# Kernel tuning notes

Measured on AMD Instinct MI355X. Metric: run time of the kernel, lower is better.

The kernel has to match this reference:

```python
import jax, jax.numpy as jnp
import numpy as np

B, H, S, D = 2, 16, 2048, 128


def setup_inputs() -> dict:
    key = jax.random.key(0)
    kq, kk, kv = jax.random.split(key, 3)
    q = jax.random.normal(kq, (B, H, S, D), dtype=jnp.float32)
    k = jax.random.normal(kk, (B, H, S, D), dtype=jnp.float32)
    v = jax.random.normal(kv, (B, H, S, D), dtype=jnp.float32)
    return {"q": q, "k": k, "v": v}


def reference(q, k, v):
    # cp_size == 1 path: causal scaled dot-product attention.
    # Identical math to the ring online-softmax accumulation collapsed to one step.
    d = q.shape[-1]
    scale = d ** -0.5
    scores = jnp.einsum("bhsd,bhtd->bhst", q, k) * scale  # (B,H,S,S)
    s = scores.shape[-1]
    causal_mask = jnp.tril(jnp.ones((s, s), dtype=bool))  # (S,S)
    scores = jnp.where(causal_mask, scores, -jnp.inf)
    probs = jax.nn.softmax(scores, axis=-1)
    return jnp.einsum("bhst,bhtd->bhsd", probs, v)
```

## Files before the change

### kernel.cpp

```cpp
#include <hip/hip_runtime.h>
#include <hip/hip_bf16.h>

constexpr int Bb = 2, Hh = 16, Ss = 2048, Dd = 128;
constexpr int BM = 64, BN = 64;
constexpr int NQT = Ss / BM;
constexpr float SCALE = 0.088388347648318447f * 1.4426950408889634f;

typedef __attribute__((ext_vector_type(8))) short bf16x8;
typedef __attribute__((ext_vector_type(4))) float f32x4;
typedef __attribute__((ext_vector_type(4))) int int4v;

__device__ __forceinline__ unsigned cvtpk(float lo, float hi) {
  unsigned r;
  asm("v_cvt_pk_bf16_f32 %0, %1, %2" : "=v"(r) : "v"(lo), "v"(hi));
  return r;
}
__device__ __forceinline__ float exp2hw(float x) {
  float r;
  asm("v_exp_f32 %0, %1" : "=v"(r) : "v"(x));
  return r;
}
__device__ __forceinline__ float fcomp(float4 f, int j) {
  return j == 0 ? f.x : (j == 1 ? f.y : (j == 2 ? f.z : f.w));
}

__global__ __launch_bounds__(256, 2)
void fa_fwd_kernel(const float* __restrict__ q, const float* __restrict__ k,
                   const float* __restrict__ v, float* __restrict__ out) {
  __shared__ __align__(16) char Klds[BN * 256];
  __shared__ __align__(16) char Vlds[Dd * 128];

  const int tid = threadIdx.x;
  const int wave = tid >> 6, lane = tid & 63, quad = lane >> 4, l16 = lane & 15;
  const int bid = blockIdx.x;
  const int bh = bid & 31;
  const int qt = (NQT - 1) - (bid >> 5);

  const float* qb = q + (size_t)bh * Ss * Dd;
  const float* kb = k + (size_t)bh * Ss * Dd;
  const float* vb = v + (size_t)bh * Ss * Dd;

  bf16x8 qf[4];
  {
    const float* qr = qb + (size_t)(qt * BM + wave * 16 + l16) * Dd + quad * 8;
    #pragma unroll
    for (int ks = 0; ks < 4; ++ks) {
      float4 a = *(const float4*)(qr + ks * 32);
      float4 b = *(const float4*)(qr + ks * 32 + 4);
      int4v t;
      t[0] = (int)cvtpk(a.x * SCALE, a.y * SCALE);
      t[1] = (int)cvtpk(a.z * SCALE, a.w * SCALE);
      t[2] = (int)cvtpk(b.x * SCALE, b.y * SCALE);
      t[3] = (int)cvtpk(b.z * SCALE, b.w * SCALE);
      qf[ks] = __builtin_bit_cast(bf16x8, t);
    }
  }

  const int krow0 = tid >> 4;
  const int kblk  = tid & 15;
  const int kswz  = kblk ^ krow0;
  const int vkg = tid >> 5;
  const int vdq = tid & 31;

  float4 ka[4], kc[4];
  float4 vr[8];

  auto load_tiles = [&](int kt) {
    const float* Kg = kb + (size_t)(kt * BN) * Dd + kblk * 8;
    #pragma unroll
    for (int i = 0; i < 4; ++i) {
      ka[i] = *(const float4*)(Kg + (size_t)(krow0 + 16 * i) * Dd);
      kc[i] = *(const float4*)(Kg + (size_t)(krow0 + 16 * i) * Dd + 4);
    }
    const float* Vg = vb + (size_t)(kt * BN + vkg * 8) * Dd + vdq * 4;
    #pragma unroll
    for (int r = 0; r < 8; ++r)
      vr[r] = *(const float4*)(Vg + (size_t)r * Dd);
  };

  auto stage_tiles = [&]() {
    #pragma unroll
    for (int i = 0; i < 4; ++i) {
      int4v t;
      t[0] = (int)cvtpk(ka[i].x, ka[i].y);
      t[1] = (int)cvtpk(ka[i].z, ka[i].w);
      t[2] = (int)cvtpk(kc[i].x, kc[i].y);
      t[3] = (int)cvtpk(kc[i].z, kc[i].w);
      *(int4v*)(Klds + (krow0 + 16 * i) * 256 + kswz * 16) = t;
    }
    #pragma unroll
    for (int j = 0; j < 4; ++j) {
      int d = vdq * 4 + j;
      int f7 = (d ^ (d >> 3)) & 7;
      int4v t;
      t[0] = (int)cvtpk(fcomp(vr[0], j), fcomp(vr[1], j));
      t[1] = (int)cvtpk(fcomp(vr[2], j), fcomp(vr[3], j));
      t[2] = (int)cvtpk(fcomp(vr[4], j), fcomp(vr[5], j));
      t[3] = (int)cvtpk(fcomp(vr[6], j), fcomp(vr[7], j));
      *(int4v*)(Vlds + d * 128 + (vkg ^ f7) * 16) = t;
    }
  };

  f32x4 o[8];
  #pragma unroll
  for (int i = 0; i < 8; ++i) o[i] = (f32x4)(0.0f);
  float mrow = -3.0e38f, lrow = 0.0f;

  load_tiles(0);
  stage_tiles();

  const int hi2 = quad >> 1;
  const int srcbase = (l16 + 32 * (quad & 1)) * 4;

  for (int kt = 0; kt <= qt; ++kt) {
    __syncthreads();
    const bool more = kt < qt;
    if (more) load_tiles(kt + 1);

    f32x4 acc[4];
    #pragma unroll
    for (int nt = 0; nt < 4; ++nt) acc[nt] = (f32x4)(0.0f);
    __builtin_amdgcn_s_setprio(1);
    #pragma unroll
    for (int ks = 0; ks < 4; ++ks) {
      #pragma unroll
      for (int nt = 0; nt < 4; ++nt) {
        int row = nt * 16 + l16;
        int bswz = (ks * 4 + quad) ^ l16;
        bf16x8 kf = *(const bf16x8*)(Klds + row * 256 + bswz * 16);
        acc[nt] = __builtin_amdgcn_mfma_f32_16x16x32_bf16(kf, qf[ks], acc[nt], 0, 0, 0);
      }
    }
    __builtin_amdgcn_s_setprio(0);

    if (kt == qt) {
      #pragma unroll
      for (int nt = 0; nt < 4; ++nt)
        #pragma unroll
        for (int r = 0; r < 4; ++r)
          if (nt * 16 + quad * 4 + r > wave * 16 + l16) acc[nt][r] = -1.0e30f;
    }

    float mx = acc[0][0];
    #pragma unroll
    for (int nt = 0; nt < 4; ++nt)
      #pragma unroll
      for (int r = 0; r < 4; ++r) mx = fmaxf(mx, acc[nt][r]);
    mx = fmaxf(mx, __shfl_xor(mx, 16, 64));
    mx = fmaxf(mx, __shfl_xor(mx, 32, 64));

    if (!__all(mx - mrow <= 8.0f)) {
      float mn = fmaxf(mrow, mx);
      float alpha = exp2hw(mrow - mn);
      mrow = mn;
      lrow *= alpha;
      #pragma unroll
      for (int r = 0; r < 4; ++r) {
        int src = (lane & 48) | (quad * 4 + r);
        float ar = __shfl(alpha, src, 64);
        #pragma unroll
        for (int dt = 0; dt < 8; ++dt) o[dt][r] *= ar;
      }
    }

    float rs = 0.f;
    #pragma unroll
    for (int nt = 0; nt < 4; ++nt)
      #pragma unroll
      for (int r = 0; r < 4; ++r) {
        float p = exp2hw(acc[nt][r] - mrow);
        acc[nt][r] = p; rs += p;
      }
    lrow += rs;

    unsigned pk0_0 = cvtpk(acc[0][0], acc[0][1]), pk0_1 = cvtpk(acc[0][2], acc[0][3]);
    unsigned pk1_0 = cvtpk(acc[1][0], acc[1][1]), pk1_1 = cvtpk(acc[1][2], acc[1][3]);
    unsigned pk2_0 = cvtpk(acc[2][0], acc[2][1]), pk2_1 = cvtpk(acc[2][2], acc[2][3]);
    unsigned pk3_0 = cvtpk(acc[3][0], acc[3][1]), pk3_1 = cvtpk(acc[3][2], acc[3][3]);

    bf16x8 pf[2];
    {
      int4v p0, p1;
      #pragma unroll
      for (int jp = 0; jp < 4; ++jp) {
        int srcb = srcbase + 64 * (jp >> 1);
        int a0 = __builtin_amdgcn_ds_bpermute(srcb, (int)((jp & 1) ? pk0_1 : pk0_0));
        int a1 = __builtin_amdgcn_ds_bpermute(srcb, (int)((jp & 1) ? pk1_1 : pk1_0));
        int a2 = __builtin_amdgcn_ds_bpermute(srcb, (int)((jp & 1) ? pk2_1 : pk2_0));
        int a3 = __builtin_amdgcn_ds_bpermute(srcb, (int)((jp & 1) ? pk3_1 : pk3_0));
        p0[jp] = hi2 ? a1 : a0;
        p1[jp] = hi2 ? a3 : a2;
      }
      pf[0] = __builtin_bit_cast(bf16x8, p0);
      pf[1] = __builtin_bit_cast(bf16x8, p1);
    }

    __builtin_amdgcn_s_setprio(1);
    #pragma unroll
    for (int ks2 = 0; ks2 < 2; ++ks2) {
      #pragma unroll
      for (int dt = 0; dt < 8; ++dt) {
        int row = dt * 16 + l16;
        int f7 = (row ^ (row >> 3)) & 7;
        int bswz = (ks2 * 4 + quad) ^ f7;
        bf16x8 vf = *(const bf16x8*)(Vlds + row * 128 + bswz * 16);
        o[dt] = __builtin_amdgcn_mfma_f32_16x16x32_bf16(pf[ks2], vf, o[dt], 0, 0, 0);
      }
    }
    __builtin_amdgcn_s_setprio(0);

    if (more) { __syncthreads(); stage_tiles(); }
  }

  lrow += __shfl_xor(lrow, 16, 64);
  lrow += __shfl_xor(lrow, 32, 64);
  float linv[4];
  #pragma unroll
  for (int r = 0; r < 4; ++r) {
    int src = (lane & 48) | (quad * 4 + r);
    linv[r] = 1.0f / __shfl(lrow, src, 64);
  }
  float* ob = out + ((size_t)bh * Ss + qt * BM + wave * 16) * Dd;
  #pragma unroll
  for (int dt = 0; dt < 8; ++dt)
    #pragma unroll
    for (int r = 0; r < 4; ++r)
      ob[(quad * 4 + r) * Dd + dt * 16 + l16] = o[dt][r] * linv[r];
}

extern "C" void kernel_launch(void* const* d_in, const int* in_sizes, int n_in,
                              void* d_out, int out_size, void* d_ws, size_t ws_size,
                              hipStream_t stream) {
  const float* q = (const float*)d_in[0];
  const float* k = (const float*)d_in[1];
  const float* v = (const float*)d_in[2];
  float* out = (float*)d_out;
  dim3 grid(Bb * Hh * NQT);
  dim3 block(256);
  hipLaunchKernelGGL(fa_fwd_kernel, grid, block, 0, stream, q, k, v, out);
}
```

Baseline: 189.2 us.

## Process two 64-row query halves per block to reuse K/V tiles

Doubles the query tile to 128 rows, so each wave keeps two sets of Q fragments, accumulators and softmax state and reuses every staged K/V tile for both halves. This halves K/V global loads and LDS staging per query row. The causal schedule is reordered to interleave heavy and light tiles, and the V prefetch is split from the K prefetch and issued later. In exchange it raises register pressure with two 8-fragment output accumulators under launch_bounds(256,2), and gives fewer blocks.

```diff
diff --git a/kernel.cpp b/kernel.cpp
--- a/kernel.cpp
+++ b/kernel.cpp
@@ -2,7 +2,7 @@
 #include <hip/hip_bf16.h>
 
 constexpr int Bb = 2, Hh = 16, Ss = 2048, Dd = 128;
-constexpr int BM = 64, BN = 64;
+constexpr int BM = 128, BN = 64;
 constexpr int NQT = Ss / BM;
 constexpr float SCALE = 0.088388347648318447f * 1.4426950408889634f;
 
@@ -34,15 +34,17 @@
   const int wave = tid >> 6, lane = tid & 63, quad = lane >> 4, l16 = lane & 15;
   const int bid = blockIdx.x;
   const int bh = bid & 31;
-  const int qt = (NQT - 1) - (bid >> 5);
+  const int r2 = bid >> 5;
+  const int qt = (r2 < 8) ? (15 - r2) : (r2 - 8);
 
   const float* qb = q + (size_t)bh * Ss * Dd;
   const float* kb = k + (size_t)bh * Ss * Dd;
   const float* vb = v + (size_t)bh * Ss * Dd;
 
-  bf16x8 qf[4];
-  {
-    const float* qr = qb + (size_t)(qt * BM + wave * 16 + l16) * Dd + quad * 8;
+  bf16x8 qf[2][4];
+  #pragma unroll
+  for (int h = 0; h < 2; ++h) {
+    const float* qr = qb + (size_t)(qt * BM + h * 64 + wave * 16 + l16) * Dd + quad * 8;
     #pragma unroll
     for (int ks = 0; ks < 4; ++ks) {
       float4 a = *(const float4*)(qr + ks * 32);
@@ -52,7 +54,7 @@
       t[1] = (int)cvtpk(a.z * SCALE, a.w * SCALE);
       t[2] = (int)cvtpk(b.x * SCALE, b.y * SCALE);
       t[3] = (int)cvtpk(b.z * SCALE, b.w * SCALE);
-      qf[ks] = __builtin_bit_cast(bf16x8, t);
+      qf[h][ks] = __builtin_bit_cast(bf16x8, t);
     }
   }
 
@@ -65,13 +67,15 @@
   float4 ka[4], kc[4];
   float4 vr[8];
 
-  auto load_tiles = [&](int kt) {
+  auto load_k = [&](int kt) {
     const float* Kg = kb + (size_t)(kt * BN) * Dd + kblk * 8;
     #pragma unroll
     for (int i = 0; i < 4; ++i) {
       ka[i] = *(const float4*)(Kg + (size_t)(krow0 + 16 * i) * Dd);
       kc[i] = *(const float4*)(Kg + (size_t)(krow0 + 16 * i) * Dd + 4);
     }
+  };
+  auto load_v = [&](int kt) {
     const float* Vg = vb + (size_t)(kt * BN + vkg * 8) * Dd + vdq * 4;
     #pragma unroll
     for (int r = 0; r < 8; ++r)
@@ -101,25 +105,30 @@
     }
   };
 
-  f32x4 o[8];
+  f32x4 o[2][8];
   #pragma unroll
-  for (int i = 0; i < 8; ++i) o[i] = (f32x4)(0.0f);
-  float mrow = -3.0e38f, lrow = 0.0f;
-
-  load_tiles(0);
+  for (int h = 0; h < 2; ++h)
+    #pragma unroll
+    for (int i = 0; i < 8; ++i) o[h][i] = (f32x4)(0.0f);
+  float mrow[2] = {-3.0e38f, -3.0e38f};
+  float lrow[2] = {0.0f, 0.0f};
+
+  load_k(0); load_v(0);
   stage_tiles();
 
   const int hi2 = quad >> 1;
   const int srcbase = (l16 + 32 * (quad & 1)) * 4;
-
-  for (int kt = 0; kt <= qt; ++kt) {
+  const int w16l16 = wave * 16 + l16;
+  const int nkt = 2 * qt + 2;
+
+  for (int kt = 0; kt < nkt; ++kt) {
     __syncthreads();
-    const bool more = kt < qt;
-    if (more) load_tiles(kt + 1);
-
-    f32x4 acc[4];
-    #pragma unroll
-    for (int nt = 0; nt < 4; ++nt) acc[nt] = (f32x4)(0.0f);
+    const bool more = kt + 1 < nkt;
+    if (more) load_k(kt + 1);
+
+    f32x4 acc[4][2];
+    #pragma unroll
+    for (int nt = 0; nt < 4; ++nt) { acc[nt][0] = (f32x4)(0.0f); acc[nt][1] = (f32x4)(0.0f); }
     __builtin_amdgcn_s_setprio(1);
     #pragma unroll
     for (int ks = 0; ks < 4; ++ks) {
@@ -128,72 +137,91 @@
         int row = nt * 16 + l16;
         int bswz = (ks * 4 + quad) ^ l16;
         bf16x8 kf = *(const bf16x8*)(Klds + row * 256 + bswz * 16);
-        acc[nt] = __builtin_amdgcn_mfma_f32_16x16x32_bf16(kf, qf[ks], acc[nt], 0, 0, 0);
+        acc[nt][0] = __builtin_amdgcn_mfma_f32_16x16x32_bf16(kf, qf[0][ks], acc[nt][0], 0, 0, 0);
+        acc[nt][1] = __builtin_amdgcn_mfma_f32_16x16x32_bf16(kf, qf[1][ks], acc[nt][1], 0, 0, 0);
       }
     }
     __builtin_amdgcn_s_setprio(0);
 
-    if (kt == qt) {
+    if (kt == nkt - 2) {
       #pragma unroll
       for (int nt = 0; nt < 4; ++nt)
         #pragma unroll
         for (int r = 0; r < 4; ++r)
-          if (nt * 16 + quad * 4 + r > wave * 16 + l16) acc[nt][r] = -1.0e30f;
-    }
-
-    float mx = acc[0][0];
-    #pragma unroll
-    for (int nt = 0; nt < 4; ++nt)
-      #pragma unroll
-      for (int r = 0; r < 4; ++r) mx = fmaxf(mx, acc[nt][r]);
-    mx = fmaxf(mx, __shfl_xor(mx, 16, 64));
-    mx = fmaxf(mx, __shfl_xor(mx, 32, 64));
-
-    if (!__all(mx - mrow <= 8.0f)) {
-      float mn = fmaxf(mrow, mx);
-      float alpha = exp2hw(mrow - mn);
-      mrow = mn;
-      lrow *= alpha;
-      #pragma unroll
-      for (int r = 0; r < 4; ++r) {
-        int src = (lane & 48) | (quad * 4 + r);
-        float ar = __shfl(alpha, src, 64);
-        #pragma unroll
-        for (int dt = 0; dt < 8; ++dt) o[dt][r] *= ar;
+          if (nt * 16 + quad * 4 + r > w16l16) acc[nt][0][r] = -1.0e30f;
+    }
+    if (kt == nkt - 1) {
+      #pragma unroll
+      for (int nt = 0; nt < 4; ++nt)
+        #pragma unroll
+        for (int r = 0; r < 4; ++r)
+          if (nt * 16 + quad * 4 + r > w16l16) acc[nt][1][r] = -1.0e30f;
+    }
+    const bool doh0 = (kt != nkt - 1);
+
+    bf16x8 pf[2][2];
+    #pragma unroll
+    for (int h = 0; h < 2; ++h) {
+      bool act = (h == 1) || doh0;
+      if (act) {
+        float mx = acc[0][h][0];
+        #pragma unroll
+        for (int nt = 0; nt < 4; ++nt)
+          #pragma unroll
+          for (int r = 0; r < 4; ++r) mx = fmaxf(mx, acc[nt][h][r]);
+        mx = fmaxf(mx, __shfl_xor(mx, 16, 64));
+        mx = fmaxf(mx, __shfl_xor(mx, 32, 64));
+
+        if (!__all(mx - mrow[h] <= 8.0f)) {
+          float mn = fmaxf(mrow[h], mx);
+          float alpha = exp2hw(mrow[h] - mn);
+          mrow[h] = mn;
+          lrow[h] *= alpha;
+          #pragma unroll
+          for (int r = 0; r < 4; ++r) {
+            int src = (lane & 48) | (quad * 4 + r);
+            float ar = __shfl(alpha, src, 64);
+            #pragma unroll
+            for (int dt = 0; dt < 8; ++dt) o[h][dt][r] *= ar;
+          }
+        }
+
+        float rs = 0.f;
+        #pragma unroll
+        for (int nt = 0; nt < 4; ++nt)
+          #pragma unroll
+          for (int r = 0; r < 4; ++r) {
+            float p = exp2hw(acc[nt][h][r] - mrow[h]);
+            acc[nt][h][r] = p; rs += p;
+          }
+        lrow[h] += rs;
+
+        unsigned pk0_0 = cvtpk(acc[0][h][0], acc[0][h][1]), pk0_1 = cvtpk(acc[0][h][2], acc[0][h][3]);
+        unsigned pk1_0 = cvtpk(acc[1][h][0], acc[1][h][1]), pk1_1 = cvtpk(acc[1][h][2], acc[1][h][3]);
+        unsigned pk2_0 = cvtpk(acc[2][h][0], acc[2][h][1]), pk2_1 = cvtpk(acc[2][h][2], acc[2][h][3]);
+        unsigned pk3_0 = cvtpk(acc[3][h][0], acc[3][h][1]), pk3_1 = cvtpk(acc[3][h][2], acc[3][h][3]);
+
+        int4v p0, p1;
+        #pragma unroll
+        for (int jp = 0; jp < 4; ++jp) {
+          int srcb = srcbase + 64 * (jp >> 1);
+          int a0 = __builtin_amdgcn_ds_bpermute(srcb, (int)((jp & 1) ? pk0_1 : pk0_0));
+          int a1 = __builtin_amdgcn_ds_bpermute(srcb, (int)((jp & 1) ? pk1_1 : pk1_0));
+          int a2 = __builtin_amdgcn_ds_bpermute(srcb, (int)((jp & 1) ? pk2_1 : pk2_0));
+          int a3 = __builtin_amdgcn_ds_bpermute(srcb, (int)((jp & 1) ? pk3_1 : pk3_0));
+          p0[jp] = hi2 ? a1 : a0;
+          p1[jp] = hi2 ? a3 : a2;
+        }
+        pf[h][0] = __builtin_bit_cast(bf16x8, p0);
+        pf[h][1] = __builtin_bit_cast(bf16x8, p1);
+      } else {
+        int4v z = (int4v)(0);
+        pf[0][0] = __builtin_bit_cast(bf16x8, z);
+        pf[0][1] = __builtin_bit_cast(bf16x8, z);
       }
     }
 
-    float rs = 0.f;
-    #pragma unroll
-    for (int nt = 0; nt < 4; ++nt)
-      #pragma unroll
-      for (int r = 0; r < 4; ++r) {
-        float p = exp2hw(acc[nt][r] - mrow);
-        acc[nt][r] = p; rs += p;
-      }
-    lrow += rs;
-
-    unsigned pk0_0 = cvtpk(acc[0][0], acc[0][1]), pk0_1 = cvtpk(acc[0][2], acc[0][3]);
-    unsigned pk1_0 = cvtpk(acc[1][0], acc[1][1]), pk1_1 = cvtpk(acc[1][2], acc[1][3]);
-    unsigned pk2_0 = cvtpk(acc[2][0], acc[2][1]), pk2_1 = cvtpk(acc[2][2], acc[2][3]);
-    unsigned pk3_0 = cvtpk(acc[3][0], acc[3][1]), pk3_1 = cvtpk(acc[3][2], acc[3][3]);
-
-    bf16x8 pf[2];
-    {
-      int4v p0, p1;
-      #pragma unroll
-      for (int jp = 0; jp < 4; ++jp) {
-        int srcb = srcbase + 64 * (jp >> 1);
-        int a0 = __builtin_amdgcn_ds_bpermute(srcb, (int)((jp & 1) ? pk0_1 : pk0_0));
-        int a1 = __builtin_amdgcn_ds_bpermute(srcb, (int)((jp & 1) ? pk1_1 : pk1_0));
-        int a2 = __builtin_amdgcn_ds_bpermute(srcb, (int)((jp & 1) ? pk2_1 : pk2_0));
-        int a3 = __builtin_amdgcn_ds_bpermute(srcb, (int)((jp & 1) ? pk3_1 : pk3_0));
-        p0[jp] = hi2 ? a1 : a0;
-        p1[jp] = hi2 ? a3 : a2;
-      }
-      pf[0] = __builtin_bit_cast(bf16x8, p0);
-      pf[1] = __builtin_bit_cast(bf16x8, p1);
-    }
+    if (more) load_v(kt + 1);
 
     __builtin_amdgcn_s_setprio(1);
     #pragma unroll
@@ -204,7 +232,8 @@
         int f7 = (row ^ (row >> 3)) & 7;
         int bswz = (ks2 * 4 + quad) ^ f7;
         bf16x8 vf = *(const bf16x8*)(Vlds + row * 128 + bswz * 16);
-        o[dt] = __builtin_amdgcn_mfma_f32_16x16x32_bf16(pf[ks2], vf, o[dt], 0, 0, 0);
+        o[0][dt] = __builtin_amdgcn_mfma_f32_16x16x32_bf16(pf[0][ks2], vf, o[0][dt], 0, 0, 0);
+        o[1][dt] = __builtin_amdgcn_mfma_f32_16x16x32_bf16(pf[1][ks2], vf, o[1][dt], 0, 0, 0);
       }
     }
     __builtin_amdgcn_s_setprio(0);
@@ -212,20 +241,24 @@
     if (more) { __syncthreads(); stage_tiles(); }
   }
 
-  lrow += __shfl_xor(lrow, 16, 64);
-  lrow += __shfl_xor(lrow, 32, 64);
-  float linv[4];
   #pragma unroll
-  for (int r = 0; r < 4; ++r) {
-    int src = (lane & 48) | (quad * 4 + r);
-    linv[r] = 1.0f / __shfl(lrow, src, 64);
+  for (int h = 0; h < 2; ++h) {
+    float lr = lrow[h];
+    lr += __shfl_xor(lr, 16, 64);
+    lr += __shfl_xor(lr, 32, 64);
+    float linv[4];
+    #pragma unroll
+    for (int r = 0; r < 4; ++r) {
+      int src = (lane & 48) | (quad * 4 + r);
+      linv[r] = 1.0f / __shfl(lr, src, 64);
+    }
+    float* ob = out + ((size_t)bh * Ss + qt * BM + h * 64 + wave * 16) * Dd;
+    #pragma unroll
+    for (int dt = 0; dt < 8; ++dt)
+      #pragma unroll
+      for (int r = 0; r < 4; ++r)
+        ob[(quad * 4 + r) * Dd + dt * 16 + l16] = o[h][dt][r] * linv[r];
   }
-  float* ob = out + ((size_t)bh * Ss + qt * BM + wave * 16) * Dd;
-  #pragma unroll
-  for (int dt = 0; dt < 8; ++dt)
-    #pragma unroll
-    for (int r = 0; r < 4; ++r)
-      ob[(quad * 4 + r) * Dd + dt * 16 + l16] = o[dt][r] * linv[r];
 }
 
 extern "C" void kernel_launch(void* const* d_in, const int* in_sizes, int n_in,
```

New measurement: 219.4 us. 16.0% more time.
